# Optimization experiments

Measured on AMD Instinct MI355X. Metric: run time of the kernel, lower is better.

Reference implementation:

```python
import jax, jax.numpy as jnp
import numpy as np
import math

NUM_BUCKETS = 32
MAX_DISTANCE = 128
N_HEADS = 16
HEAD_DIM = 64


def _relative_position_bucket(relative_position, num_buckets=NUM_BUCKETS, max_distance=MAX_DISTANCE):
    # bidirectional (encoder): half the buckets for positive positions
    nb = num_buckets // 2
    rel_buckets = (relative_position > 0).astype(jnp.int32) * nb
    rp = jnp.abs(relative_position)
    max_exact = nb // 2
    is_small = rp < max_exact
    rp_large = max_exact + (
        jnp.log(jnp.maximum(rp, 1).astype(jnp.float32) / max_exact)
        / math.log(max_distance / max_exact)
        * (nb - max_exact)
    ).astype(jnp.int32)
    rp_large = jnp.minimum(rp_large, nb - 1)
    return rel_buckets + jnp.where(is_small, rp, rp_large)


def setup_inputs() -> dict:
    key = jax.random.key(0)
    ks = jax.random.split(key, 6)
    d_model = 1024
    B, S = 4, 2048
    scale = 1.0 / math.sqrt(d_model)
    return {
        "hidden_states": jax.random.normal(ks[0], (B, S, d_model), jnp.float32),
        "Wq": jax.random.normal(ks[1], (d_model, N_HEADS * HEAD_DIM), jnp.float32) * scale,
        "Wk": jax.random.normal(ks[2], (d_model, N_HEADS * HEAD_DIM), jnp.float32) * scale,
        "Wv": jax.random.normal(ks[3], (d_model, N_HEADS * HEAD_DIM), jnp.float32) * scale,
        "Wo": jax.random.normal(ks[4], (N_HEADS * HEAD_DIM, d_model), jnp.float32) * scale,
        "rel_bias_table": jax.random.normal(ks[5], (NUM_BUCKETS, N_HEADS), jnp.float32),
    }


def reference(hidden_states, Wq, Wk, Wv, Wo, rel_bias_table):
    B, S, _ = hidden_states.shape
    # projections -> [B, H, S, hd]
    def proj(W):
        return jnp.einsum('bsd,df->bsf', hidden_states, W).reshape(B, S, N_HEADS, HEAD_DIM).transpose(0, 2, 1, 3)
    q = proj(Wq)
    k = proj(Wk)
    v = proj(Wv)

    # relative position bias: [1, H, S, S]
    ctx = jnp.arange(S)[:, None]
    mem = jnp.arange(S)[None, :]
    buckets = _relative_position_bucket(mem - ctx)  # [S, S] int32
    position_bias = rel_bias_table[buckets].transpose(2, 0, 1)[None]  # [1, H, S, S]

    # scaling = 1.0 in MT5Attention (d_kv**-0.5 baked into init elsewhere)
    attn_weights = jnp.einsum('bhqd,bhkd->bhqk', q, k) + position_bias
    attn_weights = jax.nn.softmax(attn_weights, axis=-1)
    attn_output = jnp.einsum('bhqk,bhkd->bqhd', attn_weights, v).reshape(B, S, N_HEADS * HEAD_DIM)
    attn_output = jnp.einsum('bsf,fd->bsd', attn_output, Wo)
    return attn_output, position_bias, attn_weights
```

## Files before the change

### kernel.cpp

```cpp
#include <hip/hip_runtime.h>
#include <cstdint>
#include <cmath>

#define NH 16
#define HD 64
#define SQ 2048
#define NB 4
#define DM 1024

typedef _Float16 half_t;
typedef _Float16 h8 __attribute__((ext_vector_type(8)));
typedef _Float16 h4 __attribute__((ext_vector_type(4)));
typedef float f4 __attribute__((ext_vector_type(4)));

__device__ __forceinline__ int rel_bucket(int delta) {
    int b = (delta > 0) ? 16 : 0;
    int a = (delta < 0) ? -delta : delta;
    if (a < 8) return b + a;
    int large = 8 + (int)(__logf((float)a * 0.125f) * 2.8853900817779268f);
    return b + (large < 15 ? large : 15);
}

__device__ __forceinline__ void gl_lds(const half_t* g, half_t* l) {
    __builtin_amdgcn_global_load_lds((const __attribute__((address_space(1))) unsigned int*)g,
                                     (__attribute__((address_space(3))) unsigned int*)l, 16, 0, 0);
}

__global__ __launch_bounds__(256) void prep(const float* __restrict__ X,
                                            const float* __restrict__ Wq,
                                            const float* __restrict__ Wk,
                                            const float* __restrict__ Wv,
                                            const float* __restrict__ Wo,
                                            half_t* __restrict__ Xh, half_t* __restrict__ Wqt,
                                            half_t* __restrict__ Wkt, half_t* __restrict__ Wvt,
                                            half_t* __restrict__ Wot) {
    const int id = blockIdx.x;
    if (id < 4096) {
        size_t i = ((size_t)id * 256 + threadIdx.x) * 8;
        float4 a = *(const float4*)&X[i];
        float4 b = *(const float4*)&X[i + 4];
        half_t t[8] = {(half_t)a.x, (half_t)a.y, (half_t)a.z, (half_t)a.w,
                       (half_t)b.x, (half_t)b.y, (half_t)b.z, (half_t)b.w};
        *(h8*)&Xh[i] = *(h8*)t;
        return;
    }
    __shared__ float T[64][65];
    const int t = id - 4096;
    const int which = t >> 8, tile = t & 255;
    const float* W = which == 0 ? Wq : which == 1 ? Wk : which == 2 ? Wv : Wo;
    half_t* Wt = which == 0 ? Wqt : which == 1 ? Wkt : which == 2 ? Wvt : Wot;
    const int k0 = (tile >> 4) * 64, n0 = (tile & 15) * 64;
    const int c = threadIdx.x & 63, rr = threadIdx.x >> 6;
    for (int r = rr; r < 64; r += 4) T[r][c] = W[(size_t)(k0 + r) * DM + n0 + c];
    __syncthreads();
    for (int r = rr; r < 64; r += 4) Wt[(size_t)(n0 + r) * DM + k0 + c] = (half_t)T[c][r];
}

__global__ __launch_bounds__(256) void transpose_v(const half_t* __restrict__ v,
                                                   half_t* __restrict__ vT) {
    __shared__ half_t T[64][72];
    const int bh = blockIdx.y, j0 = blockIdx.x * 64;
    const size_t base = (size_t)bh * (SQ * HD);
    const int t = threadIdx.x;
    for (int e = t; e < 512; e += 256) {
        int r = e >> 3, c = e & 7;
        *(h8*)&T[r][c * 8] = *(const h8*)&v[base + (size_t)(j0 + r) * HD + c * 8];
    }
    __syncthreads();
    const int d = t & 63, jc = t >> 6;
    half_t tmp[16];
#pragma unroll
    for (int jj = 0; jj < 16; ++jj) tmp[jj] = T[jc * 16 + jj][d];
    *(h8*)&vT[base + (size_t)d * SQ + j0 + jc * 16] = *(h8*)&tmp[0];
    *(h8*)&vT[base + (size_t)d * SQ + j0 + jc * 16 + 8] = *(h8*)&tmp[8];
}

__global__ __launch_bounds__(256) void mm_qkv(const half_t* __restrict__ A,
                                              const half_t* __restrict__ Wqt,
                                              const half_t* __restrict__ Wkt,
                                              const half_t* __restrict__ Wvt,
                                              half_t* __restrict__ qo, half_t* __restrict__ ko,
                                              half_t* __restrict__ vo) {
    const int z = blockIdx.z;
    const half_t* Bt = z == 0 ? Wqt : z == 1 ? Wkt : Wvt;
    half_t* outp = z == 0 ? qo : z == 1 ? ko : vo;
    __shared__ half_t Al[128 * 32];
    __shared__ half_t Bl[128 * 32];
    const int tid = threadIdx.x;
    const int lane = tid & 63, w = tid >> 6;
    const int wr = w >> 1, wc = w & 1;
    const int m0 = blockIdx.y * 128, n0 = blockIdx.x * 128;

    f4 acc[4][4];
#pragma unroll
    for (int i = 0; i < 4; ++i)
#pragma unroll
        for (int j = 0; j < 4; ++j) acc[i][j] = (f4){0.f, 0.f, 0.f, 0.f};

    const int kc = lane >> 4;
    const int srl = lane >> 2;
    const int sc = lane & 3;

    for (int k0 = 0; k0 < DM; k0 += 32) {
#pragma unroll
        for (int inst = 0; inst < 2; ++inst) {
            int r = w * 32 + inst * 16 + srl;
            int cg = sc ^ ((r >> 1) & 3);
            gl_lds(&A[(size_t)(m0 + r) * DM + k0 + cg * 8], &Al[(w * 32 + inst * 16) * 32]);
            gl_lds(&Bt[(size_t)(n0 + r) * DM + k0 + cg * 8], &Bl[(w * 32 + inst * 16) * 32]);
        }
        __syncthreads();
        h8 af[4], bf[4];
#pragma unroll
        for (int ms = 0; ms < 4; ++ms) {
            int r = wr * 64 + ms * 16 + (lane & 15);
            af[ms] = *(const h8*)&Al[r * 32 + ((kc ^ ((r >> 1) & 3)) * 8)];
        }
#pragma unroll
        for (int ns = 0; ns < 4; ++ns) {
            int r = wc * 64 + ns * 16 + (lane & 15);
            bf[ns] = *(const h8*)&Bl[r * 32 + ((kc ^ ((r >> 1) & 3)) * 8)];
        }
#pragma unroll
        for (int ms = 0; ms < 4; ++ms)
#pragma unroll
            for (int ns = 0; ns < 4; ++ns)
                acc[ms][ns] =
                    __builtin_amdgcn_mfma_f32_16x16x32_f16(af[ms], bf[ns], acc[ms][ns], 0, 0, 0);
        __syncthreads();
    }

#pragma unroll
    for (int ms = 0; ms < 4; ++ms)
#pragma unroll
        for (int ns = 0; ns < 4; ++ns)
#pragma unroll
            for (int reg = 0; reg < 4; ++reg) {
                int m = m0 + wr * 64 + ms * 16 + (lane >> 4) * 4 + reg;
                int n = n0 + wc * 64 + ns * 16 + (lane & 15);
                int b = m >> 11, s = m & 2047, h = n >> 6, d = n & 63;
                outp[((size_t)(b * NH + h) * SQ + s) * HD + d] = (half_t)acc[ms][ns][reg];
            }
}

__global__ __launch_bounds__(256) void mm_wo(const half_t* __restrict__ A,
                                             const half_t* __restrict__ Bt,
                                             float* __restrict__ outp) {
    __shared__ half_t Al[128 * 32];
    __shared__ half_t Bl[128 * 32];
    const int tid = threadIdx.x;
    const int lane = tid & 63, w = tid >> 6;
    const int wr = w >> 1, wc = w & 1;
    const int m0 = blockIdx.y * 128, n0 = blockIdx.x * 128;

    f4 acc[4][4];
#pragma unroll
    for (int i = 0; i < 4; ++i)
#pragma unroll
        for (int j = 0; j < 4; ++j) acc[i][j] = (f4){0.f, 0.f, 0.f, 0.f};

    const int kc = lane >> 4;
    const int srl = lane >> 2;
    const int sc = lane & 3;

    for (int k0 = 0; k0 < DM; k0 += 32) {
#pragma unroll
        for (int inst = 0; inst < 2; ++inst) {
            int r = w * 32 + inst * 16 + srl;
            int cg = sc ^ ((r >> 1) & 3);
            gl_lds(&A[(size_t)(m0 + r) * DM + k0 + cg * 8], &Al[(w * 32 + inst * 16) * 32]);
            gl_lds(&Bt[(size_t)(n0 + r) * DM + k0 + cg * 8], &Bl[(w * 32 + inst * 16) * 32]);
        }
        __syncthreads();
        h8 af[4], bf[4];
#pragma unroll
        for (int ms = 0; ms < 4; ++ms) {
            int r = wr * 64 + ms * 16 + (lane & 15);
            af[ms] = *(const h8*)&Al[r * 32 + ((kc ^ ((r >> 1) & 3)) * 8)];
        }
#pragma unroll
        for (int ns = 0; ns < 4; ++ns) {
            int r = wc * 64 + ns * 16 + (lane & 15);
            bf[ns] = *(const h8*)&Bl[r * 32 + ((kc ^ ((r >> 1) & 3)) * 8)];
        }
#pragma unroll
        for (int ms = 0; ms < 4; ++ms)
#pragma unroll
            for (int ns = 0; ns < 4; ++ns)
                acc[ms][ns] =
                    __builtin_amdgcn_mfma_f32_16x16x32_f16(af[ms], bf[ns], acc[ms][ns], 0, 0, 0);
        __syncthreads();
    }

#pragma unroll
    for (int ms = 0; ms < 4; ++ms)
#pragma unroll
        for (int ns = 0; ns < 4; ++ns)
#pragma unroll
            for (int reg = 0; reg < 4; ++reg) {
                int m = m0 + wr * 64 + ms * 16 + (lane >> 4) * 4 + reg;
                int n = n0 + wc * 64 + ns * 16 + (lane & 15);
                __builtin_nontemporal_store(acc[ms][ns][reg], &outp[(size_t)m * DM + n]);
            }
}

__global__ __launch_bounds__(256) void fused_attn(const half_t* __restrict__ q,
                                                  const half_t* __restrict__ k,
                                                  const half_t* __restrict__ vT,
                                                  const float* __restrict__ table,
                                                  float* __restrict__ attw,
                                                  half_t* __restrict__ ctx) {
    __shared__ float biasE[2176];
    __shared__ char Psm[16384];
    __shared__ half_t Kl[64 * 64];
    __shared__ half_t Vl[64 * 64];
    const int tid = threadIdx.x, lane = tid & 63, w = tid >> 6;

    const int id = blockIdx.x;
    const int idx = (id & 7) * 128 + (id >> 3);
    const int bh = idx >> 4, i0 = (idx & 15) * 128;
    const int h = bh & 15, b = bh >> 4;
    const size_t qb = (size_t)bh * (SQ * HD);
    const half_t* kb = k + qb;
    const half_t* vb = vT + qb;

    for (int t = tid; t < 2176; t += 256)
        biasE[t] = __expf(table[rel_bucket(t - i0 - 127) * NH + h]);

    h8 qf[2][2];
#pragma unroll
    for (int isub = 0; isub < 2; ++isub) {
        const half_t* qp =
            &q[qb + (size_t)(i0 + w * 32 + isub * 16 + (lane & 15)) * HD + (lane >> 4) * 8];
        qf[isub][0] = *(const h8*)qp;
        qf[isub][1] = *(const h8*)(qp + 32);
    }
    __syncthreads();

    const int sr = lane >> 3;
    const int sc = lane & 7;

    float srow[2] = {0.f, 0.f};
    for (int j0 = 0; j0 < SQ; j0 += 64) {
#pragma unroll
        for (int inst = 0; inst < 2; ++inst) {
            int r = w * 16 + inst * 8 + sr;
            gl_lds(&kb[(size_t)(j0 + r) * HD + ((sc ^ (r & 7)) * 8)], &Kl[(w * 16 + inst * 8) * 64]);
        }
        __syncthreads();
#pragma unroll
        for (int ns = 0; ns < 4; ++ns) {
            const int rr = ns * 16 + (lane & 15);
            const int kc = lane >> 4;
            h8 kf0 = *(const h8*)&Kl[rr * 64 + ((kc ^ (rr & 7)) * 8)];
            h8 kf1 = *(const h8*)&Kl[rr * 64 + (((kc + 4) ^ (rr & 7)) * 8)];
#pragma unroll
            for (int isub = 0; isub < 2; ++isub) {
                f4 z = (f4){0.f, 0.f, 0.f, 0.f};
                z = __builtin_amdgcn_mfma_f32_16x16x32_f16(kf0, qf[isub][0], z, 0, 0, 0);
                z = __builtin_amdgcn_mfma_f32_16x16x32_f16(kf1, qf[isub][1], z, 0, 0, 0);
                int u0 =
                    j0 + ns * 16 + ((lane >> 4) << 2) - (w * 32 + isub * 16 + (lane & 15)) + 127;
#pragma unroll
                for (int reg = 0; reg < 4; ++reg)
                    srow[isub] = fmaf(__expf(z[reg]), biasE[u0 + reg], srow[isub]);
            }
        }
        __syncthreads();
    }
    float sinv[2];
#pragma unroll
    for (int isub = 0; isub < 2; ++isub) {
        float s = srow[isub];
        s += __shfl_xor(s, 16);
        s += __shfl_xor(s, 32);
        sinv[isub] = 1.0f / s;
    }

    f4 o[4][2];
#pragma unroll
    for (int ns = 0; ns < 4; ++ns)
#pragma unroll
        for (int isub = 0; isub < 2; ++isub) o[ns][isub] = (f4){0.f, 0.f, 0.f, 0.f};
    const size_t awb = (size_t)bh * ((size_t)SQ * SQ);
    char* Pw = Psm + w * 4096;

    for (int j0 = 0; j0 < SQ; j0 += 64) {
#pragma unroll
        for (int inst = 0; inst < 2; ++inst) {
            int r = w * 16 + inst * 8 + sr;
            gl_lds(&kb[(size_t)(j0 + r) * HD + ((sc ^ (r & 7)) * 8)], &Kl[(w * 16 + inst * 8) * 64]);
            gl_lds(&vb[(size_t)r * SQ + j0 + ((sc ^ (r & 7)) * 8)], &Vl[(w * 16 + inst * 8) * 64]);
        }
        __syncthreads();
        f4 a[4][2];
#pragma unroll
        for (int ns = 0; ns < 4; ++ns) {
            const int rr = ns * 16 + (lane & 15);
            const int kc = lane >> 4;
            h8 kf0 = *(const h8*)&Kl[rr * 64 + ((kc ^ (rr & 7)) * 8)];
            h8 kf1 = *(const h8*)&Kl[rr * 64 + (((kc + 4) ^ (rr & 7)) * 8)];
#pragma unroll
            for (int isub = 0; isub < 2; ++isub) {
                f4 z = (f4){0.f, 0.f, 0.f, 0.f};
                z = __builtin_amdgcn_mfma_f32_16x16x32_f16(kf0, qf[isub][0], z, 0, 0, 0);
                z = __builtin_amdgcn_mfma_f32_16x16x32_f16(kf1, qf[isub][1], z, 0, 0, 0);
                a[ns][isub] = z;
            }
        }
#pragma unroll
        for (int ns = 0; ns < 4; ++ns)
#pragma unroll
            for (int isub = 0; isub < 2; ++isub) {
                const int wloc = w * 32 + isub * 16 + (lane & 15);
                const int jbase = ns * 16 + ((lane >> 4) << 2);
                const int u0 = j0 + jbase - wloc + 127;
                f4 p;
#pragma unroll
                for (int reg = 0; reg < 4; ++reg)
                    p[reg] = __expf(a[ns][isub][reg]) * biasE[u0 + reg] * sinv[isub];
                __builtin_nontemporal_store(p, (f4*)&attw[awb + (size_t)(i0 + wloc) * SQ + j0 + jbase]);
                const int iloc = isub * 16 + (lane & 15);
                h4 ph = {(half_t)p[0], (half_t)p[1], (half_t)p[2], (half_t)p[3]};
                *(h4*)&Pw[iloc * 128 + (((jbase >> 3) ^ (iloc & 7)) << 4) + ((jbase & 4) << 1)] = ph;
            }
        h8 pf[2][2];
#pragma unroll
        for (int isub = 0; isub < 2; ++isub) {
            const int iloc = isub * 16 + (lane & 15);
            pf[isub][0] = *(const h8*)&Pw[iloc * 128 + (((lane >> 4) ^ (iloc & 7)) << 4)];
            pf[isub][1] = *(const h8*)&Pw[iloc * 128 + ((((lane >> 4) + 4) ^ (iloc & 7)) << 4)];
        }
#pragma unroll
        for (int ns = 0; ns < 4; ++ns) {
            const int rr = ns * 16 + (lane & 15);
            const int kc = lane >> 4;
            h8 vf0 = *(const h8*)&Vl[rr * 64 + ((kc ^ (rr & 7)) * 8)];
            h8 vf1 = *(const h8*)&Vl[rr * 64 + (((kc + 4) ^ (rr & 7)) * 8)];
#pragma unroll
            for (int isub = 0; isub < 2; ++isub) {
                o[ns][isub] =
                    __builtin_amdgcn_mfma_f32_16x16x32_f16(pf[isub][0], vf0, o[ns][isub], 0, 0, 0);
                o[ns][isub] =
                    __builtin_amdgcn_mfma_f32_16x16x32_f16(pf[isub][1], vf1, o[ns][isub], 0, 0, 0);
            }
        }
        __syncthreads();
    }
#pragma unroll
    for (int ns = 0; ns < 4; ++ns)
#pragma unroll
        for (int isub = 0; isub < 2; ++isub)
#pragma unroll
            for (int reg = 0; reg < 4; ++reg) {
                int row = i0 + w * 32 + isub * 16 + (lane >> 4) * 4 + reg;
                int d = ns * 16 + (lane & 15);
                ctx[((size_t)(b * SQ + row)) * DM + h * HD + d] = (half_t)o[ns][isub][reg];
            }
}

__global__ __launch_bounds__(256) void bias_fill(const float* __restrict__ table,
                                                 float* __restrict__ pb) {
    __shared__ float t[512];
    const int tid = threadIdx.x;
    t[tid] = table[tid];
    t[tid + 256] = table[tid + 256];
    __syncthreads();
    const int i = blockIdx.x;
    const int h = blockIdx.y;
    const size_t base = ((size_t)h * SQ + i) * SQ;
#pragma unroll
    for (int half = 0; half < 2; ++half) {
        int j = half * 1024 + tid * 4;
        f4 o;
        o[0] = t[rel_bucket(j + 0 - i) * NH + h];
        o[1] = t[rel_bucket(j + 1 - i) * NH + h];
        o[2] = t[rel_bucket(j + 2 - i) * NH + h];
        o[3] = t[rel_bucket(j + 3 - i) * NH + h];
        __builtin_nontemporal_store(o, (f4*)&pb[base + j]);
    }
}

extern "C" void kernel_launch(void* const* d_in, const int* in_sizes, int n_in, void* d_out,
                              int out_size, void* d_ws, size_t ws_size, hipStream_t stream) {
    const float* X = (const float*)d_in[0];
    const float* Wq = (const float*)d_in[1];
    const float* Wk = (const float*)d_in[2];
    const float* Wv = (const float*)d_in[3];
    const float* Wo = (const float*)d_in[4];
    const float* tbl = (const float*)d_in[5];

    float* out = (float*)d_out;
    float* attn_out = out;
    float* pb = out + (size_t)NB * SQ * DM;
    float* attw = pb + (size_t)NH * SQ * SQ;

    const size_t need_bytes = 109051904;
    half_t* hb = (ws_size >= need_bytes) ? (half_t*)d_ws : (half_t*)pb;
    half_t* Xh = hb;
    half_t* qh = hb + 8388608;
    half_t* kh = hb + 16777216;
    half_t* vh = hb + 25165824;
    half_t* vTh = hb + 33554432;
    half_t* ctxh = hb + 41943040;
    half_t* Wqt = hb + 50331648;
    half_t* Wkt = hb + 51380224;
    half_t* Wvt = hb + 52428800;
    half_t* Wot = hb + 53477376;

    dim3 blk(256);
    prep<<<dim3(5120), blk, 0, stream>>>(X, Wq, Wk, Wv, Wo, Xh, Wqt, Wkt, Wvt, Wot);
    mm_qkv<<<dim3(8, 64, 3), blk, 0, stream>>>(Xh, Wqt, Wkt, Wvt, qh, kh, vh);
    transpose_v<<<dim3(32, 64), blk, 0, stream>>>(vh, vTh);
    fused_attn<<<dim3(1024), blk, 0, stream>>>(qh, kh, vTh, tbl, attw, ctxh);
    mm_wo<<<dim3(8, 64), blk, 0, stream>>>(ctxh, Wot, attn_out);
    bias_fill<<<dim3(SQ, NH), blk, 0, stream>>>(tbl, pb);
}
```

Before: 540.9 us.

## Double-buffer LDS tiles in the GEMM and fused attention kernels

Converts the QKV and output-projection GEMMs and both passes of the fused attention kernel to ping-pong LDS buffers. The next K/V (or A/B) tile is prefetched with global_load_lds while MFMAs run on the current tile, which removes the serialized load-then-barrier step each iteration. In the second attention pass the end-of-iteration sync becomes a partial vmcnt wait plus a raw s_barrier, so the outstanding attention-weight stores are not drained every step. This doubles tile LDS usage, which may lower occupancy. The partial wait assumes a specific count of stores issued after the prefetch loads, so correctness depends on that ordering.

```diff
diff --git a/kernel.cpp b/kernel.cpp
--- a/kernel.cpp
+++ b/kernel.cpp
@@ -84,8 +84,8 @@
     const int z = blockIdx.z;
     const half_t* Bt = z == 0 ? Wqt : z == 1 ? Wkt : Wvt;
     half_t* outp = z == 0 ? qo : z == 1 ? ko : vo;
-    __shared__ half_t Al[128 * 32];
-    __shared__ half_t Bl[128 * 32];
+    __shared__ half_t Al[2][4096];
+    __shared__ half_t Bl[2][4096];
     const int tid = threadIdx.x;
     const int lane = tid & 63, w = tid >> 6;
     const int wr = w >> 1, wc = w & 1;
@@ -101,25 +101,31 @@
     const int srl = lane >> 2;
     const int sc = lane & 3;
 
-    for (int k0 = 0; k0 < DM; k0 += 32) {
+    auto stage = [&](int buf, int k0) {
 #pragma unroll
         for (int inst = 0; inst < 2; ++inst) {
             int r = w * 32 + inst * 16 + srl;
             int cg = sc ^ ((r >> 1) & 3);
-            gl_lds(&A[(size_t)(m0 + r) * DM + k0 + cg * 8], &Al[(w * 32 + inst * 16) * 32]);
-            gl_lds(&Bt[(size_t)(n0 + r) * DM + k0 + cg * 8], &Bl[(w * 32 + inst * 16) * 32]);
-        }
-        __syncthreads();
+            gl_lds(&A[(size_t)(m0 + r) * DM + k0 + cg * 8], &Al[buf][(w * 32 + inst * 16) * 32]);
+            gl_lds(&Bt[(size_t)(n0 + r) * DM + k0 + cg * 8], &Bl[buf][(w * 32 + inst * 16) * 32]);
+        }
+    };
+
+    stage(0, 0);
+    __syncthreads();
+    int cur = 0;
+    for (int t = 0; t < 32; ++t) {
+        if (t < 31) stage(cur ^ 1, (t + 1) * 32);
         h8 af[4], bf[4];
 #pragma unroll
         for (int ms = 0; ms < 4; ++ms) {
             int r = wr * 64 + ms * 16 + (lane & 15);
-            af[ms] = *(const h8*)&Al[r * 32 + ((kc ^ ((r >> 1) & 3)) * 8)];
+            af[ms] = *(const h8*)&Al[cur][r * 32 + ((kc ^ ((r >> 1) & 3)) * 8)];
         }
 #pragma unroll
         for (int ns = 0; ns < 4; ++ns) {
             int r = wc * 64 + ns * 16 + (lane & 15);
-            bf[ns] = *(const h8*)&Bl[r * 32 + ((kc ^ ((r >> 1) & 3)) * 8)];
+            bf[ns] = *(const h8*)&Bl[cur][r * 32 + ((kc ^ ((r >> 1) & 3)) * 8)];
         }
 #pragma unroll
         for (int ms = 0; ms < 4; ++ms)
@@ -128,6 +134,7 @@
                 acc[ms][ns] =
                     __builtin_amdgcn_mfma_f32_16x16x32_f16(af[ms], bf[ns], acc[ms][ns], 0, 0, 0);
         __syncthreads();
+        cur ^= 1;
     }
 
 #pragma unroll
@@ -146,8 +153,8 @@
 __global__ __launch_bounds__(256) void mm_wo(const half_t* __restrict__ A,
                                              const half_t* __restrict__ Bt,
                                              float* __restrict__ outp) {
-    __shared__ half_t Al[128 * 32];
-    __shared__ half_t Bl[128 * 32];
+    __shared__ half_t Al[2][4096];
+    __shared__ half_t Bl[2][4096];
     const int tid = threadIdx.x;
     const int lane = tid & 63, w = tid >> 6;
     const int wr = w >> 1, wc = w & 1;
@@ -163,25 +170,31 @@
     const int srl = lane >> 2;
     const int sc = lane & 3;
 
-    for (int k0 = 0; k0 < DM; k0 += 32) {
+    auto stage = [&](int buf, int k0) {
 #pragma unroll
         for (int inst = 0; inst < 2; ++inst) {
             int r = w * 32 + inst * 16 + srl;
             int cg = sc ^ ((r >> 1) & 3);
-            gl_lds(&A[(size_t)(m0 + r) * DM + k0 + cg * 8], &Al[(w * 32 + inst * 16) * 32]);
-            gl_lds(&Bt[(size_t)(n0 + r) * DM + k0 + cg * 8], &Bl[(w * 32 + inst * 16) * 32]);
-        }
-        __syncthreads();
+            gl_lds(&A[(size_t)(m0 + r) * DM + k0 + cg * 8], &Al[buf][(w * 32 + inst * 16) * 32]);
+            gl_lds(&Bt[(size_t)(n0 + r) * DM + k0 + cg * 8], &Bl[buf][(w * 32 + inst * 16) * 32]);
+        }
+    };
+
+    stage(0, 0);
+    __syncthreads();
+    int cur = 0;
+    for (int t = 0; t < 32; ++t) {
+        if (t < 31) stage(cur ^ 1, (t + 1) * 32);
         h8 af[4], bf[4];
 #pragma unroll
         for (int ms = 0; ms < 4; ++ms) {
             int r = wr * 64 + ms * 16 + (lane & 15);
-            af[ms] = *(const h8*)&Al[r * 32 + ((kc ^ ((r >> 1) & 3)) * 8)];
+            af[ms] = *(const h8*)&Al[cur][r * 32 + ((kc ^ ((r >> 1) & 3)) * 8)];
         }
 #pragma unroll
         for (int ns = 0; ns < 4; ++ns) {
             int r = wc * 64 + ns * 16 + (lane & 15);
-            bf[ns] = *(const h8*)&Bl[r * 32 + ((kc ^ ((r >> 1) & 3)) * 8)];
+            bf[ns] = *(const h8*)&Bl[cur][r * 32 + ((kc ^ ((r >> 1) & 3)) * 8)];
         }
 #pragma unroll
         for (int ms = 0; ms < 4; ++ms)
@@ -190,6 +203,7 @@
                 acc[ms][ns] =
                     __builtin_amdgcn_mfma_f32_16x16x32_f16(af[ms], bf[ns], acc[ms][ns], 0, 0, 0);
         __syncthreads();
+        cur ^= 1;
     }
 
 #pragma unroll
@@ -212,8 +226,8 @@
                                                   half_t* __restrict__ ctx) {
     __shared__ float biasE[2176];
     __shared__ char Psm[16384];
-    __shared__ half_t Kl[64 * 64];
-    __shared__ half_t Vl[64 * 64];
+    __shared__ half_t Kl[2][4096];
+    __shared__ half_t Vl[2][4096];
     const int tid = threadIdx.x, lane = tid & 63, w = tid >> 6;
 
     const int id = blockIdx.x;
@@ -235,25 +249,40 @@
         qf[isub][0] = *(const h8*)qp;
         qf[isub][1] = *(const h8*)(qp + 32);
     }
-    __syncthreads();
 
     const int sr = lane >> 3;
     const int sc = lane & 7;
 
-    float srow[2] = {0.f, 0.f};
-    for (int j0 = 0; j0 < SQ; j0 += 64) {
+    auto stageK = [&](int buf, int j0) {
 #pragma unroll
         for (int inst = 0; inst < 2; ++inst) {
             int r = w * 16 + inst * 8 + sr;
-            gl_lds(&kb[(size_t)(j0 + r) * HD + ((sc ^ (r & 7)) * 8)], &Kl[(w * 16 + inst * 8) * 64]);
-        }
-        __syncthreads();
+            gl_lds(&kb[(size_t)(j0 + r) * HD + ((sc ^ (r & 7)) * 8)],
+                   &Kl[buf][(w * 16 + inst * 8) * 64]);
+        }
+    };
+    auto stageV = [&](int buf, int j0) {
+#pragma unroll
+        for (int inst = 0; inst < 2; ++inst) {
+            int r = w * 16 + inst * 8 + sr;
+            gl_lds(&vb[(size_t)r * SQ + j0 + ((sc ^ (r & 7)) * 8)],
+                   &Vl[buf][(w * 16 + inst * 8) * 64]);
+        }
+    };
+
+    stageK(0, 0);
+    __syncthreads();
+    float srow[2] = {0.f, 0.f};
+    int cur = 0;
+    for (int t = 0; t < 32; ++t) {
+        const int j0 = t * 64;
+        if (t < 31) stageK(cur ^ 1, j0 + 64);
 #pragma unroll
         for (int ns = 0; ns < 4; ++ns) {
             const int rr = ns * 16 + (lane & 15);
             const int kc = lane >> 4;
-            h8 kf0 = *(const h8*)&Kl[rr * 64 + ((kc ^ (rr & 7)) * 8)];
-            h8 kf1 = *(const h8*)&Kl[rr * 64 + (((kc + 4) ^ (rr & 7)) * 8)];
+            h8 kf0 = *(const h8*)&Kl[cur][rr * 64 + ((kc ^ (rr & 7)) * 8)];
+            h8 kf1 = *(const h8*)&Kl[cur][rr * 64 + (((kc + 4) ^ (rr & 7)) * 8)];
 #pragma unroll
             for (int isub = 0; isub < 2; ++isub) {
                 f4 z = (f4){0.f, 0.f, 0.f, 0.f};
@@ -267,6 +296,7 @@
             }
         }
         __syncthreads();
+        cur ^= 1;
     }
     float sinv[2];
 #pragma unroll
@@ -285,21 +315,24 @@
     const size_t awb = (size_t)bh * ((size_t)SQ * SQ);
     char* Pw = Psm + w * 4096;
 
-    for (int j0 = 0; j0 < SQ; j0 += 64) {
-#pragma unroll
-        for (int inst = 0; inst < 2; ++inst) {
-            int r = w * 16 + inst * 8 + sr;
-            gl_lds(&kb[(size_t)(j0 + r) * HD + ((sc ^ (r & 7)) * 8)], &Kl[(w * 16 + inst * 8) * 64]);
-            gl_lds(&vb[(size_t)r * SQ + j0 + ((sc ^ (r & 7)) * 8)], &Vl[(w * 16 + inst * 8) * 64]);
-        }
-        __syncthreads();
+    stageK(0, 0);
+    stageV(0, 0);
+    __syncthreads();
+    cur = 0;
+    for (int t = 0; t < 32; ++t) {
+        const int j0 = t * 64;
+        if (t < 31) {
+            stageK(cur ^ 1, j0 + 64);
+            stageV(cur ^ 1, j0 + 64);
+        }
+        __builtin_amdgcn_sched_barrier(0);
         f4 a[4][2];
 #pragma unroll
         for (int ns = 0; ns < 4; ++ns) {
             const int rr = ns * 16 + (lane & 15);
             const int kc = lane >> 4;
-            h8 kf0 = *(const h8*)&Kl[rr * 64 + ((kc ^ (rr & 7)) * 8)];
-            h8 kf1 = *(const h8*)&Kl[rr * 64 + (((kc + 4) ^ (rr & 7)) * 8)];
+            h8 kf0 = *(const h8*)&Kl[cur][rr * 64 + ((kc ^ (rr & 7)) * 8)];
+            h8 kf1 = *(const h8*)&Kl[cur][rr * 64 + (((kc + 4) ^ (rr & 7)) * 8)];
 #pragma unroll
             for (int isub = 0; isub < 2; ++isub) {
                 f4 z = (f4){0.f, 0.f, 0.f, 0.f};
@@ -319,7 +352,8 @@
 #pragma unroll
                 for (int reg = 0; reg < 4; ++reg)
                     p[reg] = __expf(a[ns][isub][reg]) * biasE[u0 + reg] * sinv[isub];
-                __builtin_nontemporal_store(p, (f4*)&attw[awb + (size_t)(i0 + wloc) * SQ + j0 + jbase]);
+                __builtin_nontemporal_store(p,
+                                            (f4*)&attw[awb + (size_t)(i0 + wloc) * SQ + j0 + jbase]);
                 const int iloc = isub * 16 + (lane & 15);
                 h4 ph = {(half_t)p[0], (half_t)p[1], (half_t)p[2], (half_t)p[3]};
                 *(h4*)&Pw[iloc * 128 + (((jbase >> 3) ^ (iloc & 7)) << 4) + ((jbase & 4) << 1)] = ph;
@@ -335,8 +369,8 @@
         for (int ns = 0; ns < 4; ++ns) {
             const int rr = ns * 16 + (lane & 15);
             const int kc = lane >> 4;
-            h8 vf0 = *(const h8*)&Vl[rr * 64 + ((kc ^ (rr & 7)) * 8)];
-            h8 vf1 = *(const h8*)&Vl[rr * 64 + (((kc + 4) ^ (rr & 7)) * 8)];
+            h8 vf0 = *(const h8*)&Vl[cur][rr * 64 + ((kc ^ (rr & 7)) * 8)];
+            h8 vf1 = *(const h8*)&Vl[cur][rr * 64 + (((kc + 4) ^ (rr & 7)) * 8)];
 #pragma unroll
             for (int isub = 0; isub < 2; ++isub) {
                 o[ns][isub] =
@@ -345,7 +379,10 @@
                     __builtin_amdgcn_mfma_f32_16x16x32_f16(pf[isub][1], vf1, o[ns][isub], 0, 0, 0);
             }
         }
-        __syncthreads();
+        asm volatile("s_waitcnt vmcnt(8)" ::: "memory");
+        __builtin_amdgcn_s_barrier();
+        __builtin_amdgcn_sched_barrier(0);
+        cur ^= 1;
     }
 #pragma unroll
     for (int ns = 0; ns < 4; ++ns)
```

New measurement: 550.3 us. Within noise of the previous version (+1.7%).
